# Optimization experiments

Hardware: AMD Instinct MI355X
Metric: run time of the kernel (lower is better)

The kernel has to match this reference:

```python
import jax, jax.numpy as jnp
import numpy as np

M, K, N = 4096, 4096, 11008  # tokens, in_features, out_features


def setup_inputs() -> dict:
    key = jax.random.key(0)
    k1, k2, k3, k4 = jax.random.split(key, 4)
    x = jax.random.normal(k1, (M, K), dtype=jnp.float32)
    weight = jax.random.randint(k2, (N, K), -128, 128).astype(jnp.int8)
    # per-output-channel scale, small positive values as from real quantization
    weight_scale = (jax.random.uniform(k3, (N,), dtype=jnp.float32) * 0.01 + 1e-4)
    bias = jax.random.normal(k4, (N,), dtype=jnp.float32)
    return {"x": x, "weight": weight, "weight_scale": weight_scale, "bias": bias}


def reference(x, weight, weight_scale, bias):
    # Dynamic per-token symmetric quantization of activations to int8.
    x_scale = jnp.max(jnp.abs(x), axis=-1, keepdims=True) / 127.0  # [M, 1]
    x_scale = jnp.maximum(x_scale, 1e-8)
    x_q = jnp.clip(jnp.round(x / x_scale), -128, 127).astype(jnp.int8)  # [M, K]
    acc = jax.lax.dot_general(
        x_q, weight,
        dimension_numbers=(((1,), (1,)), ((), ())),
        preferred_element_type=jnp.int32,
    )
    # Dequantize: per-token activation scale * per-channel weight scale, add bias.
    out = acc.astype(jnp.float32) * x_scale * weight_scale[None, :] + bias[None, :]
    return out
```

## Files before the change

kernel.cpp:

```cpp
#include <hip/hip_runtime.h>
#include <stdint.h>

#define M_DIM 4096
#define K_DIM 4096
#define N_DIM 11008

typedef int v4i __attribute__((ext_vector_type(4)));

#define LDSP(p) ((__attribute__((address_space(3))) void*)(uintptr_t)(p))
#define GLBP(p) ((__attribute__((address_space(1))) void*)(uintptr_t)(p))

__global__ __launch_bounds__(256) void quant_rows(const float* __restrict__ x,
                                                  int8_t* __restrict__ xq,
                                                  float* __restrict__ xs_out) {
    const int row = blockIdx.x;
    const int t = threadIdx.x;
    const float4* xr = (const float4*)(x + (size_t)row * K_DIM);

    float4 v[4];
    float amax = 0.0f;
#pragma unroll
    for (int r = 0; r < 4; ++r) {
        v[r] = xr[t + r * 256];
        amax = fmaxf(amax, fmaxf(fmaxf(fabsf(v[r].x), fabsf(v[r].y)),
                                 fmaxf(fabsf(v[r].z), fabsf(v[r].w))));
    }
#pragma unroll
    for (int off = 32; off > 0; off >>= 1)
        amax = fmaxf(amax, __shfl_xor(amax, off));

    __shared__ float smax[4];
    if ((t & 63) == 0) smax[t >> 6] = amax;
    __syncthreads();
    amax = fmaxf(fmaxf(smax[0], smax[1]), fmaxf(smax[2], smax[3]));

    const float xs = fmaxf(amax / 127.0f, 1e-8f);
    if (t == 0) xs_out[row] = xs;

    int* qo = (int*)(xq + (size_t)row * K_DIM);
#pragma unroll
    for (int r = 0; r < 4; ++r) {
        int q0 = (int)rintf(v[r].x / xs);
        int q1 = (int)rintf(v[r].y / xs);
        int q2 = (int)rintf(v[r].z / xs);
        int q3 = (int)rintf(v[r].w / xs);
        q0 = min(127, max(-128, q0));
        q1 = min(127, max(-128, q1));
        q2 = min(127, max(-128, q2));
        q3 = min(127, max(-128, q3));
        int packed = (q0 & 255) | ((q1 & 255) << 8) | ((q2 & 255) << 16) | (q3 << 24);
        qo[t + r * 256] = packed;
    }
}

__global__ __launch_bounds__(256) void prep_weight(const void* __restrict__ wraw,
                                                   int8_t* __restrict__ w8) {
    const int* wi = (const int*)wraw;
    int c = 0;
#pragma unroll
    for (int i = 0; i < 64; ++i) {
        int w = wi[i];
        c += (w >= -128 && w <= 127) ? 1 : 0;
    }
    const size_t tid = (size_t)blockIdx.x * 256 + threadIdx.x;
    if (c >= 32) {
        union { int4 v; char b[16]; } o;
#pragma unroll
        for (int g = 0; g < 4; ++g) {
            int4 w = ((const int4*)wraw)[tid * 4 + g];
            o.b[g * 4 + 0] = (char)w.x;
            o.b[g * 4 + 1] = (char)w.y;
            o.b[g * 4 + 2] = (char)w.z;
            o.b[g * 4 + 3] = (char)w.w;
        }
        ((int4*)w8)[tid] = o.v;
    } else {
        ((int4*)w8)[tid] = ((const int4*)wraw)[tid];
    }
}

__global__ __launch_bounds__(512, 2) void w8a8_gemm(const int8_t* __restrict__ xq,
                                                    const float* __restrict__ xscale,
                                                    const int8_t* __restrict__ wgt,
                                                    const float* __restrict__ wscale,
                                                    const float* __restrict__ bias,
                                                    float* __restrict__ out) {
    __shared__ __align__(16) int8_t lds_a[2][256 * 128];
    __shared__ __align__(16) int8_t lds_b[2][256 * 128];

    const int t = threadIdx.x;
    const int lane = t & 63;
    const int wave = t >> 6;
    const int wm = wave >> 2;
    const int wn = wave & 3;
    const int quad = lane >> 4;
    const int l15 = lane & 15;

    const int wg = blockIdx.x;
    const int swz = (wg & 7) * 86 + (wg >> 3);
    const int bm = swz / 43;
    const int bn = swz % 43;

    const int8_t* pa = xq + (size_t)bm * 256 * K_DIM;
    const int8_t* pb = wgt + (size_t)bn * 256 * K_DIM;

    const int srow = t >> 3;
    const size_t soff = (size_t)srow * K_DIM + (size_t)(((t & 7) ^ (srow & 7)) << 4);
    const size_t g1 = (size_t)64 * K_DIM;
    const size_t h1 = (size_t)128 * K_DIM;

#define STAGE_HALF(gb, lb)                                                               \
    do {                                                                                 \
        __builtin_amdgcn_global_load_lds(GLBP((gb) + soff), LDSP((lb) + t * 16), 16, 0, 0); \
        __builtin_amdgcn_global_load_lds(GLBP((gb) + soff + g1), LDSP((lb) + 8192 + t * 16), 16, 0, 0); \
    } while (0)

    int abase[2], bbase[2];
#pragma unroll
    for (int ks = 0; ks < 2; ++ks) {
        const int ar = wm * 128 + l15;
        abase[ks] = ar * 128 + (((ks * 4 + quad) ^ (l15 & 7)) << 4);
        const int br = wn * 64 + l15;
        bbase[ks] = br * 128 + (((ks * 4 + quad) ^ (l15 & 7)) << 4);
    }

    int8_t* la0 = &lds_a[0][0];
    int8_t* la1 = &lds_a[1][0];
    int8_t* lb0 = &lds_b[0][0];
    int8_t* lb1 = &lds_b[1][0];

    v4i acc[8][4] = {};
    v4i af[8], bf[8];

#define READ_B(c)                                                     \
    _Pragma("unroll") for (int j = 0; j < 4; ++j) {                   \
        bf[j] = *(const v4i*)(&lds_b[c][bbase[0] + j * 2048]);        \
        bf[4 + j] = *(const v4i*)(&lds_b[c][bbase[1] + j * 2048]);    \
    }
#define READ_A4(c, ks, i0)                                            \
    _Pragma("unroll") for (int i = 0; i < 4; ++i)                     \
        af[(i0) + i] = *(const v4i*)(&lds_a[c][abase[ks] + ((i0) + i) * 2048]);
#define MFMA16(A0, B0)                                                \
    _Pragma("unroll") for (int i = 0; i < 4; ++i)                     \
    _Pragma("unroll") for (int j = 0; j < 4; ++j)                     \
        acc[(A0) + i][j] = __builtin_amdgcn_mfma_i32_16x16x64_i8(     \
            af[(A0) + i], bf[(B0) + j], acc[(A0) + i][j], 0, 0, 0);
#define PH_PRE                                                        \
    __builtin_amdgcn_s_barrier();                                     \
    asm volatile("s_waitcnt lgkmcnt(0)" ::: "memory");                \
    __builtin_amdgcn_s_setprio(1);
#define PH_POST                                                       \
    __builtin_amdgcn_s_setprio(0);                                    \
    __builtin_amdgcn_s_barrier();

    STAGE_HALF(pa, la0);
    STAGE_HALF(pa + h1, la0 + 16384);
    STAGE_HALF(pb, lb0);
    STAGE_HALF(pb + h1, lb0 + 16384);
    STAGE_HALF(pa + 128, la1);
    STAGE_HALF(pa + 128 + h1, la1 + 16384);
    STAGE_HALF(pb + 128, lb1);
    STAGE_HALF(pb + 128 + h1, lb1 + 16384);
    asm volatile("s_waitcnt vmcnt(8)" ::: "memory");
    __builtin_amdgcn_s_barrier();

#pragma unroll 1
    for (int p = 0; p < 16; ++p) {
        const bool st = (p < 15);
        const int8_t* qa = pa + (size_t)(2 * p + 2) * 128;
        const int8_t* qb = pb + (size_t)(2 * p + 2) * 128;

        READ_B(0);
        READ_A4(0, 0, 0);
        PH_PRE; MFMA16(0, 0); PH_POST;
        READ_A4(0, 0, 4);
        if (st) STAGE_HALF(qb, lb0);
        PH_PRE; MFMA16(4, 0); PH_POST;
        READ_A4(0, 1, 0);
        READ_A4(0, 1, 4);
        if (st) STAGE_HALF(qb + h1, lb0 + 16384);
        PH_PRE; MFMA16(0, 4); PH_POST;
        if (st) {
            STAGE_HALF(qa, la0);
            asm volatile("s_waitcnt vmcnt(6)" ::: "memory");
        } else {
            asm volatile("s_waitcnt vmcnt(0)" ::: "memory");
        }
        PH_PRE; MFMA16(4, 4); PH_POST;

        READ_B(1);
        READ_A4(1, 0, 0);
        if (st) STAGE_HALF(qa + h1, la0 + 16384);
        PH_PRE; MFMA16(0, 0); PH_POST;
        READ_A4(1, 0, 4);
        if (st) STAGE_HALF(qb + 128, lb1);
        PH_PRE; MFMA16(4, 0); PH_POST;
        READ_A4(1, 1, 0);
        READ_A4(1, 1, 4);
        if (st) STAGE_HALF(qb + 128 + h1, lb1 + 16384);
        PH_PRE; MFMA16(0, 4); PH_POST;
        if (st) {
            STAGE_HALF(qa + 128, la1);
            STAGE_HALF(qa + 128 + h1, la1 + 16384);
            asm volatile("s_waitcnt vmcnt(6)" ::: "memory");
        }
        PH_PRE; MFMA16(4, 4); PH_POST;
    }

    float wsc[4], bi[4];
#pragma unroll
    for (int j = 0; j < 4; ++j) {
        const int cc = bn * 256 + wn * 64 + j * 16 + l15;
        wsc[j] = wscale[cc];
        bi[j] = bias[cc];
    }
#pragma unroll
    for (int i = 0; i < 8; ++i) {
        const int m0 = bm * 256 + wm * 128 + i * 16 + quad * 4;
        const float4 xs4 = *(const float4*)(xscale + m0);
        const float xsv[4] = {xs4.x, xs4.y, xs4.z, xs4.w};
#pragma unroll
        for (int r = 0; r < 4; ++r) {
            const size_t off = (size_t)(m0 + r) * N_DIM + (size_t)bn * 256 + wn * 64 + l15;
#pragma unroll
            for (int j = 0; j < 4; ++j) {
                out[off + j * 16] = (float)acc[i][j][r] * xsv[r] * wsc[j] + bi[j];
            }
        }
    }
}

extern "C" void kernel_launch(void* const* d_in, const int* in_sizes, int n_in,
                              void* d_out, int out_size, void* d_ws, size_t ws_size,
                              hipStream_t stream) {
    const float* x = (const float*)d_in[0];
    const void* wraw = (const void*)d_in[1];
    const float* wscale = (const float*)d_in[2];
    const float* bias = (const float*)d_in[3];
    float* out = (float*)d_out;

    int8_t* w8 = (int8_t*)d_ws;
    int8_t* xq = (int8_t*)d_ws + (size_t)N_DIM * K_DIM;
    float* xs = (float*)((char*)d_ws + (size_t)N_DIM * K_DIM + (size_t)M_DIM * K_DIM);

    quant_rows<<<M_DIM, 256, 0, stream>>>(x, xq, xs);
    prep_weight<<<(N_DIM * (K_DIM / 16)) / 256, 256, 0, stream>>>(wraw, w8);
    w8a8_gemm<<<688, 512, 0, stream>>>(xq, xs, w8, wscale, bias, out);
}
```

Measured before the change: 509.7 us.

## Triple-buffer A tiles and restructure K-loop into two-phase per-tile schedule

Reworks the GEMM main loop so A uses a three-slot LDS ring while B stays double-buffered. Each 128-wide K tile is processed in two MFMA phases over all eight A fragments, with prefetches issued further ahead. The loop is unrolled by six with a peeled tail. The workgroup-to-tile mapping is also changed so each XCD handles two adjacent M-block rows across all N-blocks. The goal is to hide global load latency better and improve L2 reuse, at the cost of more LDS per block (160KB), which may limit occupancy, and more live A fragment registers.

```diff
diff --git a/kernel.cpp b/kernel.cpp
--- a/kernel.cpp
+++ b/kernel.cpp
@@ -85,8 +85,8 @@
                                                     const float* __restrict__ wscale,
                                                     const float* __restrict__ bias,
                                                     float* __restrict__ out) {
-    __shared__ __align__(16) int8_t lds_a[2][256 * 128];
-    __shared__ __align__(16) int8_t lds_b[2][256 * 128];
+    __shared__ __align__(16) int8_t lds_a[3][32768];
+    __shared__ __align__(16) int8_t lds_b[2][32768];
 
     const int t = threadIdx.x;
     const int lane = t & 63;
@@ -97,22 +97,24 @@
     const int l15 = lane & 15;
 
     const int wg = blockIdx.x;
-    const int swz = (wg & 7) * 86 + (wg >> 3);
-    const int bm = swz / 43;
-    const int bn = swz % 43;
+    const int xcd = wg & 7;
+    const int u = wg >> 3;
+    const int bm = 2 * xcd + (u & 1);
+    const int bn = u >> 1;
 
     const int8_t* pa = xq + (size_t)bm * 256 * K_DIM;
     const int8_t* pb = wgt + (size_t)bn * 256 * K_DIM;
 
     const int srow = t >> 3;
     const size_t soff = (size_t)srow * K_DIM + (size_t)(((t & 7) ^ (srow & 7)) << 4);
-    const size_t g1 = (size_t)64 * K_DIM;
-    const size_t h1 = (size_t)128 * K_DIM;
-
-#define STAGE_HALF(gb, lb)                                                               \
-    do {                                                                                 \
-        __builtin_amdgcn_global_load_lds(GLBP((gb) + soff), LDSP((lb) + t * 16), 16, 0, 0); \
-        __builtin_amdgcn_global_load_lds(GLBP((gb) + soff + g1), LDSP((lb) + 8192 + t * 16), 16, 0, 0); \
+    const size_t g64 = (size_t)64 * K_DIM;
+
+#define STAGE_TILE(gb, lb)                                                                   \
+    do {                                                                                     \
+        __builtin_amdgcn_global_load_lds(GLBP((gb) + soff), LDSP((lb) + t * 16), 16, 0, 0);  \
+        __builtin_amdgcn_global_load_lds(GLBP((gb) + soff + g64), LDSP((lb) + 8192 + t * 16), 16, 0, 0); \
+        __builtin_amdgcn_global_load_lds(GLBP((gb) + soff + 2 * g64), LDSP((lb) + 16384 + t * 16), 16, 0, 0); \
+        __builtin_amdgcn_global_load_lds(GLBP((gb) + soff + 3 * g64), LDSP((lb) + 24576 + t * 16), 16, 0, 0); \
     } while (0)
 
     int abase[2], bbase[2];
@@ -124,27 +126,22 @@
         bbase[ks] = br * 128 + (((ks * 4 + quad) ^ (l15 & 7)) << 4);
     }
 
-    int8_t* la0 = &lds_a[0][0];
-    int8_t* la1 = &lds_a[1][0];
-    int8_t* lb0 = &lds_b[0][0];
-    int8_t* lb1 = &lds_b[1][0];
-
     v4i acc[8][4] = {};
     v4i af[8], bf[8];
 
-#define READ_B(c)                                                     \
+#define READ_B8(SB)                                                   \
     _Pragma("unroll") for (int j = 0; j < 4; ++j) {                   \
-        bf[j] = *(const v4i*)(&lds_b[c][bbase[0] + j * 2048]);        \
-        bf[4 + j] = *(const v4i*)(&lds_b[c][bbase[1] + j * 2048]);    \
-    }
-#define READ_A4(c, ks, i0)                                            \
-    _Pragma("unroll") for (int i = 0; i < 4; ++i)                     \
-        af[(i0) + i] = *(const v4i*)(&lds_a[c][abase[ks] + ((i0) + i) * 2048]);
-#define MFMA16(A0, B0)                                                \
-    _Pragma("unroll") for (int i = 0; i < 4; ++i)                     \
+        bf[j] = *(const v4i*)(&lds_b[SB][bbase[0] + j * 2048]);       \
+        bf[4 + j] = *(const v4i*)(&lds_b[SB][bbase[1] + j * 2048]);   \
+    }
+#define READ_A8(SA, KS)                                               \
+    _Pragma("unroll") for (int i = 0; i < 8; ++i)                     \
+        af[i] = *(const v4i*)(&lds_a[SA][abase[KS] + i * 2048]);
+#define MFMA16(B0)                                                    \
+    _Pragma("unroll") for (int i = 0; i < 8; ++i)                     \
     _Pragma("unroll") for (int j = 0; j < 4; ++j)                     \
-        acc[(A0) + i][j] = __builtin_amdgcn_mfma_i32_16x16x64_i8(     \
-            af[(A0) + i], bf[(B0) + j], acc[(A0) + i][j], 0, 0, 0);
+        acc[i][j] = __builtin_amdgcn_mfma_i32_16x16x64_i8(            \
+            af[i], bf[(B0) + j], acc[i][j], 0, 0, 0);
 #define PH_PRE                                                        \
     __builtin_amdgcn_s_barrier();                                     \
     asm volatile("s_waitcnt lgkmcnt(0)" ::: "memory");                \
@@ -153,59 +150,51 @@
     __builtin_amdgcn_s_setprio(0);                                    \
     __builtin_amdgcn_s_barrier();
 
-    STAGE_HALF(pa, la0);
-    STAGE_HALF(pa + h1, la0 + 16384);
-    STAGE_HALF(pb, lb0);
-    STAGE_HALF(pb + h1, lb0 + 16384);
-    STAGE_HALF(pa + 128, la1);
-    STAGE_HALF(pa + 128 + h1, la1 + 16384);
-    STAGE_HALF(pb + 128, lb1);
-    STAGE_HALF(pb + 128 + h1, lb1 + 16384);
+    STAGE_TILE(pa, &lds_a[0][0]);
+    STAGE_TILE(pb, &lds_b[0][0]);
+    STAGE_TILE(pa + 128, &lds_a[1][0]);
+    STAGE_TILE(pb + 128, &lds_b[1][0]);
     asm volatile("s_waitcnt vmcnt(8)" ::: "memory");
     __builtin_amdgcn_s_barrier();
 
+#define DO_TILE(U)                                                       \
+    {                                                                    \
+        constexpr int SA = (U) % 3;                                      \
+        constexpr int SB = (U) % 2;                                      \
+        constexpr int SA2 = ((U) + 2) % 3;                               \
+        const size_t k2 = (size_t)(t0 + (U) + 2) * 128;                  \
+                                                                \
+        READ_B8(SB);                                                     \
+        READ_A8(SA, 0);                                                  \
+        STAGE_TILE(pa + k2, &lds_a[SA2][0]);                             \
+        PH_PRE; MFMA16(0); PH_POST;                                      \
+                                                                \
+        READ_A8(SA, 1);                                                  \
+        STAGE_TILE(pb + k2, &lds_b[SB][0]);                              \
+        asm volatile("s_waitcnt vmcnt(8)" ::: "memory");                 \
+        PH_PRE; MFMA16(4); PH_POST;                                      \
+    }
+
 #pragma unroll 1
-    for (int p = 0; p < 16; ++p) {
-        const bool st = (p < 15);
-        const int8_t* qa = pa + (size_t)(2 * p + 2) * 128;
-        const int8_t* qb = pb + (size_t)(2 * p + 2) * 128;
-
-        READ_B(0);
-        READ_A4(0, 0, 0);
-        PH_PRE; MFMA16(0, 0); PH_POST;
-        READ_A4(0, 0, 4);
-        if (st) STAGE_HALF(qb, lb0);
-        PH_PRE; MFMA16(4, 0); PH_POST;
-        READ_A4(0, 1, 0);
-        READ_A4(0, 1, 4);
-        if (st) STAGE_HALF(qb + h1, lb0 + 16384);
-        PH_PRE; MFMA16(0, 4); PH_POST;
-        if (st) {
-            STAGE_HALF(qa, la0);
-            asm volatile("s_waitcnt vmcnt(6)" ::: "memory");
-        } else {
-            asm volatile("s_waitcnt vmcnt(0)" ::: "memory");
-        }
-        PH_PRE; MFMA16(4, 4); PH_POST;
-
-        READ_B(1);
-        READ_A4(1, 0, 0);
-        if (st) STAGE_HALF(qa + h1, la0 + 16384);
-        PH_PRE; MFMA16(0, 0); PH_POST;
-        READ_A4(1, 0, 4);
-        if (st) STAGE_HALF(qb + 128, lb1);
-        PH_PRE; MFMA16(4, 0); PH_POST;
-        READ_A4(1, 1, 0);
-        READ_A4(1, 1, 4);
-        if (st) STAGE_HALF(qb + 128 + h1, lb1 + 16384);
-        PH_PRE; MFMA16(0, 4); PH_POST;
-        if (st) {
-            STAGE_HALF(qa + 128, la1);
-            STAGE_HALF(qa + 128 + h1, la1 + 16384);
-            asm volatile("s_waitcnt vmcnt(6)" ::: "memory");
-        }
-        PH_PRE; MFMA16(4, 4); PH_POST;
-    }
+    for (int t0 = 0; t0 < 30; t0 += 6) {
+        DO_TILE(0)
+        DO_TILE(1)
+        DO_TILE(2)
+        DO_TILE(3)
+        DO_TILE(4)
+        DO_TILE(5)
+    }
+    READ_B8(0);
+    READ_A8(0, 0);
+    PH_PRE; MFMA16(0); PH_POST;
+    READ_A8(0, 1);
+    asm volatile("s_waitcnt vmcnt(0)" ::: "memory");
+    PH_PRE; MFMA16(4); PH_POST;
+    READ_B8(1);
+    READ_A8(1, 0);
+    PH_PRE; MFMA16(0); PH_POST;
+    READ_A8(1, 1);
+    PH_PRE; MFMA16(4); PH_POST;
 
     float wsc[4], bi[4];
 #pragma unroll
```

New measurement: 494.6 us. 3.0% less time.
